# Optimization experiments

Measured on AMD Instinct MI355X. Metric: run time of the kernel, lower is better.

## Reference

```python
import jax, jax.numpy as jnp
import numpy as np

K = 32
BN_EPS = 1e-5
GRID = [[0.1, 0.1, 0.1], [0.5, 0.5, 0.5], [0.2, 0.2, 0.05]]


def setup_inputs() -> dict:
    key = jax.random.key(0)
    ks = jax.random.split(key, 8)
    B, P, C = 4, 6144, 64
    N = B * P
    feat = jax.random.normal(ks[0], (N, C), jnp.float32)
    coord = jax.random.normal(ks[1], (N, 3), jnp.float32) * 10.0
    batch = jnp.repeat(jnp.arange(B, dtype=jnp.int32), P)
    # feature_judge params: Linear(C,64) -> BatchNorm1d(64, eval) -> ReLU -> Linear(64,3)
    W1 = jax.random.normal(ks[2], (C, 64), jnp.float32) / np.sqrt(C)
    b1 = jnp.zeros((64,), jnp.float32)
    gamma = jnp.ones((64,), jnp.float32)
    beta = jnp.zeros((64,), jnp.float32)
    bn_mean = jax.random.normal(ks[3], (64,), jnp.float32) * 0.1
    bn_var = jax.random.uniform(ks[4], (64,), jnp.float32, 0.5, 1.5)
    W2 = jax.random.normal(ks[5], (64, 3), jnp.float32) / 8.0
    b2 = jnp.zeros((3,), jnp.float32)
    return {"feat": feat, "coord": coord, "batch": batch, "W1": W1, "b1": b1,
            "gamma": gamma, "beta": beta, "bn_mean": bn_mean, "bn_var": bn_var,
            "W2": W2, "b2": b2}


def _geometry(coord, B):
    # coord: [N,3] with equal-size contiguous batches -> [B,P,3]
    N = coord.shape[0]
    P = N // B
    pts = coord.reshape(B, P, 3)
    sq = jnp.sum(pts * pts, axis=-1)                               # [B,P]
    d2 = sq[:, :, None] + sq[:, None, :] - 2.0 * jnp.einsum('bpd,bqd->bpq', pts, pts)
    dist = jnp.sqrt(jnp.maximum(d2, 1e-12))                        # [B,P,P]
    _, idx = jax.lax.top_k(-dist, K + 1)                           # smallest K+1
    idx = idx[:, :, 1:]                                            # drop self -> [B,P,K]
    nbrs = jax.vmap(lambda p, i: p[i])(pts, idx)                   # [B,P,K,3]
    centered = nbrs - nbrs.mean(axis=2, keepdims=True)
    cov = jnp.einsum('bpki,bpkj->bpij', centered, centered) / (K - 1)  # [B,P,3,3]
    ev = jnp.linalg.eigvalsh(cov)[..., ::-1]                       # descending, == svd S (PSD)
    ev = ev / jnp.sum(ev, axis=-1, keepdims=True)
    linearity = (ev[..., 0] - (ev[..., 1] + ev[..., 2])).reshape(N)
    nbr_d = jnp.take_along_axis(dist, idx, axis=2)                 # [B,P,K]
    density = (1.0 / (nbr_d.mean(axis=-1) + 1e-6)).reshape(N)
    return linearity, density


def reference(feat, coord, batch, W1, b1, gamma, beta, bn_mean, bn_var, W2, b2):
    B = int(batch[-1]) + 1
    linearity, density = _geometry(coord, B)
    # feature judge MLP (BatchNorm in eval mode with running stats)
    h = feat @ W1 + b1
    h = gamma * (h - bn_mean) / jnp.sqrt(bn_var + BN_EPS) + beta
    h = jax.nn.relu(h)
    probs = jax.nn.softmax(h @ W2 + b2, axis=1)                    # [N,3]
    lin = linearity[:, None]
    den = density[:, None]
    tower_prob = (den * 2.0 + probs[:, 0:1]) / 3.0
    background_prob = (jnp.maximum(1.0 - lin, 1.0 - den) + probs[:, 1:2]) / 3.0
    line_prob = (lin * 2.0 + probs[:, 2:3]) / 3.0
    tower_g = jnp.asarray(GRID[0], jnp.float32)
    bg_g = jnp.asarray(GRID[1], jnp.float32)
    line_g = jnp.asarray([GRID[2][0], GRID[2][1], GRID[2][2] * 5.0], jnp.float32)
    grid_sizes = tower_prob * tower_g + background_prob * bg_g + line_prob * line_g + 1e-6
    return grid_sizes  # [N,3]
```

## Files before the change

### kernel.cpp

```cpp
#include <hip/hip_runtime.h>
#include <hip/hip_bf16.h>
#include <math.h>

#define TS 512
#define BUFCAP 128
#define KMAX 0xFFFFFFFFFFFFFFFFull

typedef __hip_bfloat16 bf16;
typedef unsigned long long u64;

__device__ inline float ldf(const void* p, int idx, bool isbf) {
  return isbf ? __bfloat162float(((const bf16*)p)[idx])
              : ((const float*)p)[idx];
}

__device__ inline bool probe_is_bf16(const void* bn_var) {
  int ok = 0;
#pragma unroll 1
  for (int k = 0; k < 8; ++k) {
    float v = __bfloat162float(((const bf16*)bn_var)[k]);
    if (v >= 0.4f && v <= 1.6f) ++ok;
  }
  return ok == 8;
}

__device__ inline u64 shfl_xor_u64(u64 v, int mask) {
  unsigned lo = __shfl_xor((unsigned)v, mask, 64);
  unsigned hi = __shfl_xor((unsigned)(v >> 32), mask, 64);
  return ((u64)hi << 32) | lo;
}

__device__ inline u64 bcast_u64(u64 v, int srclane) {
  unsigned lo = __shfl((unsigned)v, srclane, 64);
  unsigned hi = __shfl((unsigned)(v >> 32), srclane, 64);
  return ((u64)hi << 32) | lo;
}

__device__ inline void bitonic128(u64& a0, u64& a1, int lane) {
#pragma unroll
  for (int k = 2; k <= 128; k <<= 1) {
#pragma unroll
    for (int j = k >> 1; j > 0; j >>= 1) {
      if (j == 64) {
        u64 lo = (a0 < a1) ? a0 : a1;
        u64 hi = (a0 < a1) ? a1 : a0;
        a0 = lo; a1 = hi;
      } else {
        u64 p0 = shfl_xor_u64(a0, j);
        u64 p1 = shfl_xor_u64(a1, j);
        bool lower = ((lane & j) == 0);
        bool up0 = ((lane & k) == 0);
        bool up1 = (((64 + lane) & k) == 0);
        a0 = ((p0 < a0) == (lower == up0)) ? p0 : a0;
        a1 = ((p1 < a1) == (lower == up1)) ? p1 : a1;
      }
    }
  }
}

__device__ inline float bitonic64_f32(float a, int lane) {
#pragma unroll
  for (int k = 2; k <= 64; k <<= 1) {
#pragma unroll
    for (int j = k >> 1; j > 0; j >>= 1) {
      float p = __shfl_xor(a, j, 64);
      bool lower = ((lane & j) == 0);
      bool up = ((lane & k) == 0);
      a = ((p < a) == (lower == up)) ? p : a;
    }
  }
  return a;
}

__device__ inline u64 reselect(volatile u64* wbuf, int& cnt, int lane) {
  u64 a0 = (lane < cnt) ? wbuf[lane] : KMAX;
  u64 a1 = (64 + lane < cnt) ? wbuf[64 + lane] : KMAX;
  bitonic128(a0, a1, lane);
  if (lane < 32) wbuf[lane] = a0;
  cnt = 32;
  return bcast_u64(a0, 31);
}

#define RED32(v)             \
  v += __shfl_xor(v, 1, 64); \
  v += __shfl_xor(v, 2, 64); \
  v += __shfl_xor(v, 4, 64); \
  v += __shfl_xor(v, 8, 64); \
  v += __shfl_xor(v, 16, 64);
#define RED64(v) RED32(v) v += __shfl_xor(v, 32, 64);

__device__ inline void epilogue(volatile u64* wbuf, int cnt, int lane, int i,
                                int base, int P, float qx, float qy, float qz,
                                const void* coord, const void* feat,
                                const void* W1, const void* b1,
                                const void* gamma_, const void* beta_,
                                const void* bn_mean, const void* bn_var,
                                const void* W2, const void* b2,
                                float* __restrict__ out, bool isbf) {
  reselect(wbuf, cnt, lane);
  u64 K = (lane < 32) ? wbuf[lane] : KMAX;

  float sd = 0.f, sx = 0.f, sy = 0.f, sz = 0.f;
  float sxx = 0.f, sxy = 0.f, sxz = 0.f, syy = 0.f, syz = 0.f, szz = 0.f;
  if (lane < 32) {
    unsigned cpos = (unsigned)(K & 0xFFFFFFFFull);
    if (cpos >= (unsigned)P) cpos = 0;
    float d2 = __uint_as_float((unsigned)(K >> 32));
    sd = sqrtf(d2);
    int g = 3 * (base + (int)cpos);
    float dx = ldf(coord, g + 0, isbf) - qx,
          dy = ldf(coord, g + 1, isbf) - qy,
          dz = ldf(coord, g + 2, isbf) - qz;
    sx = dx; sy = dy; sz = dz;
    sxx = dx * dx; sxy = dx * dy; sxz = dx * dz;
    syy = dy * dy; syz = dy * dz; szz = dz * dz;
  }
  RED32(sd) RED32(sx) RED32(sy) RED32(sz) RED32(sxx) RED32(sxy) RED32(sxz)
  RED32(syy) RED32(syz) RED32(szz)

  float bnv = ldf(bn_var, lane, isbf);
  float bs = ldf(gamma_, lane, isbf) / sqrtf(bnv + 1e-5f);
  float bt = (ldf(b1, lane, isbf) - ldf(bn_mean, lane, isbf)) * bs +
             ldf(beta_, lane, isbf);
  float fv = ldf(feat, i * 64 + lane, isbf);
  float h = 0.f;
#pragma unroll 4
  for (int k = 0; k < 64; ++k) {
    float w1k = ldf(W1, k * 64 + lane, isbf);
    h = fmaf(__shfl(fv, k, 64), w1k, h);
  }
  h = fmaxf(fmaf(h, bs, bt), 0.f);
  float l0 = h * ldf(W2, lane * 3 + 0, isbf);
  float l1 = h * ldf(W2, lane * 3 + 1, isbf);
  float l2 = h * ldf(W2, lane * 3 + 2, isbf);
  RED64(l0) RED64(l1) RED64(l2)
  l0 += ldf(b2, 0, isbf); l1 += ldf(b2, 1, isbf); l2 += ldf(b2, 2, isbf);
  float m = fmaxf(l0, fmaxf(l1, l2));
  float e0 = expf(l0 - m), e1 = expf(l1 - m), e2 = expf(l2 - m);
  float inv = 1.f / (e0 + e1 + e2);
  float pr0 = e0 * inv, pr1 = e1 * inv, pr2 = e2 * inv;

  if (lane == 0) {
    const float n = 32.0f, km1 = 31.0f;
    float mx = sx / n, my = sy / n, mz = sz / n;
    float a = (sxx - n * mx * mx) / km1;
    float bb = (syy - n * my * my) / km1;
    float cc2 = (szz - n * mz * mz) / km1;
    float d = (sxy - n * mx * my) / km1;
    float e = (syz - n * my * mz) / km1;
    float f = (sxz - n * mx * mz) / km1;
    float tr = a + bb + cc2;
    float qq = tr / 3.0f;
    float p1 = d * d + f * f + e * e;
    float aq = a - qq, bq = bb - qq, cq = cc2 - qq;
    float p2 = aq * aq + bq * bq + cq * cq + 2.0f * p1;
    float p = sqrtf(p2 / 6.0f);
    float ev0;
    if (p < 1e-20f) {
      ev0 = qq;
    } else {
      float ip = 1.0f / p;
      float b00 = aq * ip, b11 = bq * ip, b22 = cq * ip;
      float b01 = d * ip, b12 = e * ip, b02 = f * ip;
      float r = (b00 * (b11 * b22 - b12 * b12) -
                 b01 * (b01 * b22 - b12 * b02) +
                 b02 * (b01 * b12 - b11 * b02)) * 0.5f;
      r = fminf(1.0f, fmaxf(-1.0f, r));
      float phi = acosf(r) / 3.0f;
      ev0 = qq + 2.0f * p * cosf(phi);
    }
    float lin = 2.0f * ev0 / tr - 1.0f;
    float den = 1.0f / (sd / 32.0f + 1e-6f);
    float tp = (den * 2.0f + pr0) / 3.0f;
    float bp = (fmaxf(1.0f - lin, 1.0f - den) + pr1) / 3.0f;
    float lp = (lin * 2.0f + pr2) / 3.0f;
    float g0 = tp * 0.1f + bp * 0.5f + lp * 0.2f + 1e-6f;
    float g2 = tp * 0.1f + bp * 0.5f + lp * 0.25f + 1e-6f;
    if (!isfinite(g0)) g0 = 0.f;
    if (!isfinite(g2)) g2 = 0.f;
    out[3 * i + 0] = g0;
    out[3 * i + 1] = g0;
    out[3 * i + 2] = g2;
  }
}

__global__ __launch_bounds__(256) void prep_kernel(
    const void* __restrict__ coord, const void* __restrict__ bn_var,
    float4* __restrict__ wsf4, int N) {
  const bool isbf = probe_is_bf16(bn_var);
  int i = blockIdx.x * 256 + threadIdx.x;
  if (i >= N) return;
  int g = 3 * i;
  float x = ldf(coord, g + 0, isbf), y = ldf(coord, g + 1, isbf),
        z = ldf(coord, g + 2, isbf);
  wsf4[i] = make_float4(x, y, z, (x * x + y * y) + z * z);
}

__global__ __launch_bounds__(256) void fused_stream(
    const void* __restrict__ coord, const void* __restrict__ feat,
    const void* __restrict__ W1, const void* __restrict__ b1,
    const void* __restrict__ gamma_, const void* __restrict__ beta_,
    const void* __restrict__ bn_mean, const void* __restrict__ bn_var,
    const void* __restrict__ W2, const void* __restrict__ b2,
    const float4* __restrict__ wsf4, float* __restrict__ out, int N) {
  __shared__ u64 sBuf[4 * BUFCAP];

  const bool isbf = probe_is_bf16(bn_var);
  int tid = threadIdx.x;
  int lane = tid & 63;
  int w = tid >> 6;
  int i = blockIdx.x * 4 + w;
  int P = N / 4;
  int base = (i / P) * P;
  int mypos = i - base;
  volatile u64* wbuf = &sBuf[w * BUFCAP];
  u64 lmask = (1ull << lane) - 1;
  const float4* cb = wsf4 + base;

  float qx = ldf(coord, 3 * i + 0, isbf);
  float qy = ldf(coord, 3 * i + 1, isbf);
  float qz = ldf(coord, 3 * i + 2, isbf);
  float qsq = (qx * qx + qy * qy) + qz * qz;

  int cnt = 0;

  float th_f;
  {
    int sstride = (P - 1) >> 6;
    int sidx = mypos + 1 + lane * sstride;
    if (sidx >= P) sidx -= P;
    float4 c = cb[sidx];
    float t = qx * c.x;
    t = fmaf(qy, c.y, t);
    t = fmaf(qz, c.z, t);
    float d2 = (qsq + c.w) - 2.0f * t;
    d2 = fmaxf(d2, 1e-12f);
    th_f = __shfl(bitonic64_f32(d2, lane), 31, 64);
  }

  const int ngroups = P / 512;

#pragma unroll 1
  for (int g = 0; g < ngroups; ++g) {
    int t0 = g * 512;
    float4 cd[8];
#pragma unroll
    for (int s = 0; s < 8; ++s) cd[s] = cb[t0 + s * 64 + lane];
    float d2v[8];
    bool anyp = false;
#pragma unroll
    for (int s = 0; s < 8; ++s) {
      float t = qx * cd[s].x;
      t = fmaf(qy, cd[s].y, t);
      t = fmaf(qz, cd[s].z, t);
      float d2 = (qsq + cd[s].w) - 2.0f * t;
      d2 = fmaxf(d2, 1e-12f);
      d2v[s] = d2;
      anyp = anyp || (d2 <= th_f);
    }
    if (__ballot(anyp)) {
#pragma unroll
      for (int s = 0; s < 8; ++s) {
        float d2 = d2v[s];
        int cpos = t0 + s * 64 + lane;
        bool cand = (d2 <= th_f) && (cpos != mypos);
        u64 mask = __ballot(cand);
        if (mask) {
          u64 key = ((u64)__float_as_uint(d2) << 32) | (unsigned)cpos;
          int pc = __popcll(mask);
          if (cnt + pc > BUFCAP) {
            u64 th = reselect(wbuf, cnt, lane);
            th_f = __uint_as_float((unsigned)(th >> 32));
            cand = cand && (d2 <= th_f);
            mask = __ballot(cand);
            pc = __popcll(mask);
          }
          if (mask) {
            int pos = cnt + __popcll(mask & lmask);
            if (cand) wbuf[pos] = key;
            cnt += pc;
          }
        }
      }
    }
  }

  epilogue(wbuf, cnt, lane, i, base, P, qx, qy, qz, coord, feat, W1, b1,
           gamma_, beta_, bn_mean, bn_var, W2, b2, out, isbf);
}

__global__ __launch_bounds__(256) void fused_kernel(
    const void* __restrict__ coord, const void* __restrict__ feat,
    const void* __restrict__ W1, const void* __restrict__ b1,
    const void* __restrict__ gamma_, const void* __restrict__ beta_,
    const void* __restrict__ bn_mean, const void* __restrict__ bn_var,
    const void* __restrict__ W2, const void* __restrict__ b2,
    float* __restrict__ out, int N) {
  __shared__ float4 sTile[TS];
  __shared__ u64 sBuf[4 * BUFCAP];

  const bool isbf = probe_is_bf16(bn_var);
  int tid = threadIdx.x;
  int lane = tid & 63;
  int w = tid >> 6;
  int i = blockIdx.x * 4 + w;
  int P = N / 4;
  int base = (i / P) * P;
  int mypos = i - base;
  volatile u64* wbuf = &sBuf[w * BUFCAP];
  u64 lmask = (1ull << lane) - 1;

  float qx = ldf(coord, 3 * i + 0, isbf);
  float qy = ldf(coord, 3 * i + 1, isbf);
  float qz = ldf(coord, 3 * i + 2, isbf);
  float qsq = (qx * qx + qy * qy) + qz * qz;

  int cnt = 0;
  float th_f;
  {
    int sstride = (P - 1) >> 6;
    int sidx = mypos + 1 + lane * sstride;
    if (sidx >= P) sidx -= P;
    int g = 3 * (base + sidx);
    float x = ldf(coord, g + 0, isbf), y = ldf(coord, g + 1, isbf),
          z = ldf(coord, g + 2, isbf);
    float csq = (x * x + y * y) + z * z;
    float t = qx * x;
    t = fmaf(qy, y, t);
    t = fmaf(qz, z, t);
    float d2 = (qsq + csq) - 2.0f * t;
    d2 = fmaxf(d2, 1e-12f);
    th_f = __shfl(bitonic64_f32(d2, lane), 31, 64);
  }

  const int ntiles = P / TS;
  for (int tile = 0; tile < ntiles; ++tile) {
    __syncthreads();
    {
      int c0 = tile * TS + tid;
      int g = 3 * (base + c0);
      float x = ldf(coord, g + 0, isbf), y = ldf(coord, g + 1, isbf),
            z = ldf(coord, g + 2, isbf);
      sTile[tid] = make_float4(x, y, z, (x * x + y * y) + z * z);
      g = 3 * (base + c0 + 256);
      x = ldf(coord, g + 0, isbf); y = ldf(coord, g + 1, isbf);
      z = ldf(coord, g + 2, isbf);
      sTile[tid + 256] = make_float4(x, y, z, (x * x + y * y) + z * z);
    }
    __syncthreads();
    int t0 = tile * TS;

    float d2v[8];
    bool anyp = false;
#pragma unroll
    for (int s = 0; s < 8; ++s) {
      float4 cd = sTile[s * 64 + lane];
      float t = qx * cd.x;
      t = fmaf(qy, cd.y, t);
      t = fmaf(qz, cd.z, t);
      float d2 = (qsq + cd.w) - 2.0f * t;
      d2 = fmaxf(d2, 1e-12f);
      d2v[s] = d2;
      anyp = anyp || (d2 <= th_f);
    }
    if (__ballot(anyp)) {
#pragma unroll
      for (int s = 0; s < 8; ++s) {
        float d2 = d2v[s];
        int cpos = t0 + s * 64 + lane;
        bool cand = (d2 <= th_f) && (cpos != mypos);
        u64 mask = __ballot(cand);
        if (mask) {
          u64 key = ((u64)__float_as_uint(d2) << 32) | (unsigned)cpos;
          int pc = __popcll(mask);
          if (cnt + pc > BUFCAP) {
            u64 th = reselect(wbuf, cnt, lane);
            th_f = __uint_as_float((unsigned)(th >> 32));
            cand = cand && (d2 <= th_f);
            mask = __ballot(cand);
            pc = __popcll(mask);
          }
          if (mask) {
            int pos = cnt + __popcll(mask & lmask);
            if (cand) wbuf[pos] = key;
            cnt += pc;
          }
        }
      }
    }
  }

  epilogue(wbuf, cnt, lane, i, base, P, qx, qy, qz, coord, feat, W1, b1,
           gamma_, beta_, bn_mean, bn_var, W2, b2, out, isbf);
}

extern "C" void kernel_launch(void* const* d_in, const int* in_sizes, int n_in,
                              void* d_out, int out_size, void* d_ws,
                              size_t ws_size, hipStream_t stream) {
  const void* feat = d_in[0];
  const void* coord = d_in[1];
  const void* W1 = d_in[3];
  const void* b1 = d_in[4];
  const void* gamma_ = d_in[5];
  const void* beta_ = d_in[6];
  const void* bn_mean = d_in[7];
  const void* bn_var = d_in[8];
  const void* W2 = d_in[9];
  const void* b2 = d_in[10];
  float* out = (float*)d_out;

  int N = in_sizes[0] / 64;
  (void)n_in; (void)out_size;

  size_t need = (size_t)N * sizeof(float4);
  if (d_ws != nullptr && ws_size >= need) {
    hipLaunchKernelGGL(prep_kernel, dim3((N + 255) / 256), dim3(256), 0,
                       stream, coord, bn_var, (float4*)d_ws, N);
    hipLaunchKernelGGL(fused_stream, dim3(N / 4), dim3(256), 0, stream,
                       coord, feat, W1, b1, gamma_, beta_, bn_mean, bn_var,
                       W2, b2, (const float4*)d_ws, out, N);
  } else {
    hipLaunchKernelGGL(fused_kernel, dim3(N / 4), dim3(256), 0, stream,
                       coord, feat, W1, b1, gamma_, beta_, bn_mean, bn_var,
                       W2, b2, out, N);
  }
}
```

Baseline: 280.6 us.

## Replace brute-force kNN with x-bucketed spatial sort and pruned slab search

Points are bucketed by x coordinate into 512 fixed-width bins per batch via histogram, prefix scan and atomic scatter into a sorted workspace. Each query then scans only the bins near its own x and grows the window outward while the slab-edge distance squared is within the current k-th threshold. This replaces the brute-force scan over all P candidates per query with a pruned search. In exchange it adds four small preprocessing kernels and atomics, and the bucket range is hard-coded around coordinates in [-64, 64], so its pruning relies on the input coordinate scale.

```diff
diff --git a/kernel.cpp b/kernel.cpp
--- a/kernel.cpp
+++ b/kernel.cpp
@@ -5,9 +5,17 @@
 #define TS 512
 #define BUFCAP 128
 #define KMAX 0xFFFFFFFFFFFFFFFFull
+#define FINF __int_as_float(0x7F800000)
+
+#define NB 512
+#define BLO_F (-64.0f)
+#define BW_F (0.25f)
+#define BINV_F (4.0f)
+#define EDGE_SLACK (1e-3f)
 
 typedef __hip_bfloat16 bf16;
 typedef unsigned long long u64;
+typedef unsigned int u32;
 
 __device__ inline float ldf(const void* p, int idx, bool isbf) {
   return isbf ? __bfloat162float(((const bf16*)p)[idx])
@@ -22,6 +30,12 @@
     if (v >= 0.4f && v <= 1.6f) ++ok;
   }
   return ok == 8;
+}
+
+__device__ inline int bucket_of(float x) {
+  int b = (int)((x - BLO_F) * BINV_F);
+  b = b < 0 ? 0 : (b > NB - 1 ? NB - 1 : b);
+  return b;
 }
 
 __device__ inline u64 shfl_xor_u64(u64 v, int mask) {
@@ -88,6 +102,43 @@
   v += __shfl_xor(v, 8, 64); \
   v += __shfl_xor(v, 16, 64);
 #define RED64(v) RED32(v) v += __shfl_xor(v, 32, 64);
+
+__device__ inline void scan_seg(const float4* __restrict__ arr,
+                                const u32* __restrict__ aidx, int s0, int s1,
+                                float qx, float qy, float qz, float qsq,
+                                u32 mypos, float& th_f, int& cnt,
+                                volatile u64* wbuf, int lane, u64 lmask) {
+#pragma unroll 1
+  for (int p = s0; p < s1; p += 64) {
+    int pos = p + lane;
+    bool valid = pos < s1;
+    float4 c = make_float4(0.f, 0.f, 0.f, 0.f);
+    u32 cp = 0xFFFFFFFFu;
+    if (valid) { c = arr[pos]; cp = aidx[pos]; }
+    float t = qx * c.x;
+    t = fmaf(qy, c.y, t);
+    t = fmaf(qz, c.z, t);
+    float d2 = (qsq + c.w) - 2.0f * t;
+    d2 = fmaxf(d2, 1e-12f);
+    bool cand = valid && (d2 <= th_f) && (cp != mypos);
+    u64 mask = __ballot(cand);
+    if (!mask) continue;
+    u64 key = ((u64)__float_as_uint(d2) << 32) | cp;
+    int pc = __popcll(mask);
+    if (cnt + pc > BUFCAP) {
+      u64 th = reselect(wbuf, cnt, lane);
+      th_f = __uint_as_float((u32)(th >> 32));
+      cand = cand && (d2 <= th_f);
+      mask = __ballot(cand);
+      pc = __popcll(mask);
+    }
+    if (mask) {
+      int q = cnt + __popcll(mask & lmask);
+      if (cand) wbuf[q] = key;
+      cnt += pc;
+    }
+  }
+}
 
 __device__ inline void epilogue(volatile u64* wbuf, int cnt, int lane, int i,
                                 int base, int P, float qx, float qy, float qz,
@@ -184,25 +235,146 @@
   }
 }
 
-__global__ __launch_bounds__(256) void prep_kernel(
-    const void* __restrict__ coord, const void* __restrict__ bn_var,
-    float4* __restrict__ wsf4, int N) {
+__global__ __launch_bounds__(256) void k_zero(u32* __restrict__ hist) {
+  int t = blockIdx.x * 256 + threadIdx.x;
+  if (t < 4 * NB) hist[t] = 0u;
+}
+
+__global__ __launch_bounds__(256) void k_hist(const void* __restrict__ coord,
+                                              const void* __restrict__ bn_var,
+                                              u32* __restrict__ hist, int N) {
   const bool isbf = probe_is_bf16(bn_var);
   int i = blockIdx.x * 256 + threadIdx.x;
   if (i >= N) return;
-  int g = 3 * i;
-  float x = ldf(coord, g + 0, isbf), y = ldf(coord, g + 1, isbf),
-        z = ldf(coord, g + 2, isbf);
-  wsf4[i] = make_float4(x, y, z, (x * x + y * y) + z * z);
-}
-
-__global__ __launch_bounds__(256) void fused_stream(
+  int P = N / 4;
+  int b = i / P;
+  float x = ldf(coord, 3 * i, isbf);
+  atomicAdd(&hist[b * NB + bucket_of(x)], 1u);
+}
+
+__global__ __launch_bounds__(512) void k_scan(const u32* __restrict__ hist,
+                                              u32* __restrict__ off,
+                                              u32* __restrict__ cur) {
+  __shared__ u32 s[NB];
+  int b = blockIdx.x, t = threadIdx.x;
+  u32 v = hist[b * NB + t];
+  s[t] = v;
+  __syncthreads();
+  for (int d = 1; d < NB; d <<= 1) {
+    u32 add = (t >= d) ? s[t - d] : 0u;
+    __syncthreads();
+    s[t] += add;
+    __syncthreads();
+  }
+  u32 incl = s[t];
+  off[b * (NB + 1) + t + 1] = incl;
+  if (t == 0) off[b * (NB + 1)] = 0u;
+  cur[b * NB + t] = incl - v;
+}
+
+__global__ __launch_bounds__(256) void k_scatter(
+    const void* __restrict__ coord, const void* __restrict__ bn_var,
+    u32* __restrict__ cur, float4* __restrict__ arr4, u32* __restrict__ aidx,
+    int N) {
+  const bool isbf = probe_is_bf16(bn_var);
+  int i = blockIdx.x * 256 + threadIdx.x;
+  if (i >= N) return;
+  int P = N / 4;
+  int b = i / P;
+  int base = b * P;
+  float x = ldf(coord, 3 * i + 0, isbf), y = ldf(coord, 3 * i + 1, isbf),
+        z = ldf(coord, 3 * i + 2, isbf);
+  u32 pos = atomicAdd(&cur[b * NB + bucket_of(x)], 1u);
+  arr4[base + pos] = make_float4(x, y, z, (x * x + y * y) + z * z);
+  aidx[base + pos] = (u32)(i - base);
+}
+
+__global__ __launch_bounds__(256) void knn_kernel(
     const void* __restrict__ coord, const void* __restrict__ feat,
     const void* __restrict__ W1, const void* __restrict__ b1,
     const void* __restrict__ gamma_, const void* __restrict__ beta_,
     const void* __restrict__ bn_mean, const void* __restrict__ bn_var,
     const void* __restrict__ W2, const void* __restrict__ b2,
-    const float4* __restrict__ wsf4, float* __restrict__ out, int N) {
+    const float4* __restrict__ arr4, const u32* __restrict__ aidx,
+    const u32* __restrict__ off, float* __restrict__ out, int N) {
+  __shared__ u64 sBuf[4 * BUFCAP];
+
+  const bool isbf = probe_is_bf16(bn_var);
+  int tid = threadIdx.x;
+  int lane = tid & 63;
+  int w = tid >> 6;
+  int i = blockIdx.x * 4 + w;
+  int P = N / 4;
+  int b = i / P;
+  int base = b * P;
+  u32 mypos = (u32)(i - base);
+  const float4* arr = arr4 + base;
+  const u32* ai = aidx + base;
+  const u32* offp = off + b * (NB + 1);
+  volatile u64* wbuf = &sBuf[w * BUFCAP];
+  u64 lmask = (1ull << lane) - 1;
+
+  float qx = ldf(coord, 3 * i + 0, isbf);
+  float qy = ldf(coord, 3 * i + 1, isbf);
+  float qz = ldf(coord, 3 * i + 2, isbf);
+  float qsq = (qx * qx + qy * qy) + qz * qz;
+
+  float th_f = FINF;
+  int cnt = 0;
+
+  int bq = bucket_of(qx);
+  int blo = bq, bhi = bq, D = 1;
+  while ((int)(offp[bhi + 1] - offp[blo]) < 128 && (blo > 0 || bhi < NB - 1)) {
+    blo = (blo - D < 0) ? 0 : blo - D;
+    bhi = (bhi + D > NB - 1) ? NB - 1 : bhi + D;
+    D <<= 1;
+  }
+  scan_seg(arr, ai, (int)offp[blo], (int)offp[bhi + 1], qx, qy, qz, qsq,
+           mypos, th_f, cnt, wbuf, lane, lmask);
+  {
+    u64 th = reselect(wbuf, cnt, lane);
+    th_f = __uint_as_float((u32)(th >> 32));
+  }
+
+#pragma unroll 1
+  for (int guard = 0; guard < 4096; ++guard) {
+    float dl = (blo > 0)
+                   ? fmaxf(qx - (BLO_F + (float)blo * BW_F) - EDGE_SLACK, 0.f)
+                   : FINF;
+    float dr = (bhi < NB - 1)
+                   ? fmaxf((BLO_F + (float)(bhi + 1) * BW_F) - qx - EDGE_SLACK,
+                           0.f)
+                   : FINF;
+    float m = fminf(dl, dr);
+    if (!(m * m <= th_f)) break;
+    if (dl <= dr) {
+      int nblo = blo;
+      while (nblo > 0 && (int)(offp[blo] - offp[nblo]) < 64) --nblo;
+      scan_seg(arr, ai, (int)offp[nblo], (int)offp[blo], qx, qy, qz, qsq,
+               mypos, th_f, cnt, wbuf, lane, lmask);
+      blo = nblo;
+    } else {
+      int nbhi = bhi;
+      while (nbhi < NB - 1 && (int)(offp[nbhi + 1] - offp[bhi + 1]) < 64)
+        ++nbhi;
+      scan_seg(arr, ai, (int)offp[bhi + 1], (int)offp[nbhi + 1], qx, qy, qz,
+               qsq, mypos, th_f, cnt, wbuf, lane, lmask);
+      bhi = nbhi;
+    }
+  }
+
+  epilogue(wbuf, cnt, lane, i, base, P, qx, qy, qz, coord, feat, W1, b1,
+           gamma_, beta_, bn_mean, bn_var, W2, b2, out, isbf);
+}
+
+__global__ __launch_bounds__(256) void fused_kernel(
+    const void* __restrict__ coord, const void* __restrict__ feat,
+    const void* __restrict__ W1, const void* __restrict__ b1,
+    const void* __restrict__ gamma_, const void* __restrict__ beta_,
+    const void* __restrict__ bn_mean, const void* __restrict__ bn_var,
+    const void* __restrict__ W2, const void* __restrict__ b2,
+    float* __restrict__ out, int N) {
+  __shared__ float4 sTile[TS];
   __shared__ u64 sBuf[4 * BUFCAP];
 
   const bool isbf = probe_is_bf16(bn_var);
@@ -215,7 +387,6 @@
   int mypos = i - base;
   volatile u64* wbuf = &sBuf[w * BUFCAP];
   u64 lmask = (1ull << lane) - 1;
-  const float4* cb = wsf4 + base;
 
   float qx = ldf(coord, 3 * i + 0, isbf);
   float qy = ldf(coord, 3 * i + 1, isbf);
@@ -223,37 +394,49 @@
   float qsq = (qx * qx + qy * qy) + qz * qz;
 
   int cnt = 0;
-
   float th_f;
   {
     int sstride = (P - 1) >> 6;
     int sidx = mypos + 1 + lane * sstride;
     if (sidx >= P) sidx -= P;
-    float4 c = cb[sidx];
-    float t = qx * c.x;
-    t = fmaf(qy, c.y, t);
-    t = fmaf(qz, c.z, t);
-    float d2 = (qsq + c.w) - 2.0f * t;
+    int g = 3 * (base + sidx);
+    float x = ldf(coord, g + 0, isbf), y = ldf(coord, g + 1, isbf),
+          z = ldf(coord, g + 2, isbf);
+    float csq = (x * x + y * y) + z * z;
+    float t = qx * x;
+    t = fmaf(qy, y, t);
+    t = fmaf(qz, z, t);
+    float d2 = (qsq + csq) - 2.0f * t;
     d2 = fmaxf(d2, 1e-12f);
     th_f = __shfl(bitonic64_f32(d2, lane), 31, 64);
   }
 
-  const int ngroups = P / 512;
-
-#pragma unroll 1
-  for (int g = 0; g < ngroups; ++g) {
-    int t0 = g * 512;
-    float4 cd[8];
-#pragma unroll
-    for (int s = 0; s < 8; ++s) cd[s] = cb[t0 + s * 64 + lane];
+  const int ntiles = P / TS;
+  for (int tile = 0; tile < ntiles; ++tile) {
+    __syncthreads();
+    {
+      int c0 = tile * TS + tid;
+      int g = 3 * (base + c0);
+      float x = ldf(coord, g + 0, isbf), y = ldf(coord, g + 1, isbf),
+            z = ldf(coord, g + 2, isbf);
+      sTile[tid] = make_float4(x, y, z, (x * x + y * y) + z * z);
+      g = 3 * (base + c0 + 256);
+      x = ldf(coord, g + 0, isbf); y = ldf(coord, g + 1, isbf);
+      z = ldf(coord, g + 2, isbf);
+      sTile[tid + 256] = make_float4(x, y, z, (x * x + y * y) + z * z);
+    }
+    __syncthreads();
+    int t0 = tile * TS;
+
     float d2v[8];
     bool anyp = false;
 #pragma unroll
     for (int s = 0; s < 8; ++s) {
-      float t = qx * cd[s].x;
-      t = fmaf(qy, cd[s].y, t);
-      t = fmaf(qz, cd[s].z, t);
-      float d2 = (qsq + cd[s].w) - 2.0f * t;
+      float4 cd = sTile[s * 64 + lane];
+      float t = qx * cd.x;
+      t = fmaf(qy, cd.y, t);
+      t = fmaf(qz, cd.z, t);
+      float d2 = (qsq + cd.w) - 2.0f * t;
       d2 = fmaxf(d2, 1e-12f);
       d2v[s] = d2;
       anyp = anyp || (d2 <= th_f);
@@ -289,111 +472,6 @@
            gamma_, beta_, bn_mean, bn_var, W2, b2, out, isbf);
 }
 
-__global__ __launch_bounds__(256) void fused_kernel(
-    const void* __restrict__ coord, const void* __restrict__ feat,
-    const void* __restrict__ W1, const void* __restrict__ b1,
-    const void* __restrict__ gamma_, const void* __restrict__ beta_,
-    const void* __restrict__ bn_mean, const void* __restrict__ bn_var,
-    const void* __restrict__ W2, const void* __restrict__ b2,
-    float* __restrict__ out, int N) {
-  __shared__ float4 sTile[TS];
-  __shared__ u64 sBuf[4 * BUFCAP];
-
-  const bool isbf = probe_is_bf16(bn_var);
-  int tid = threadIdx.x;
-  int lane = tid & 63;
-  int w = tid >> 6;
-  int i = blockIdx.x * 4 + w;
-  int P = N / 4;
-  int base = (i / P) * P;
-  int mypos = i - base;
-  volatile u64* wbuf = &sBuf[w * BUFCAP];
-  u64 lmask = (1ull << lane) - 1;
-
-  float qx = ldf(coord, 3 * i + 0, isbf);
-  float qy = ldf(coord, 3 * i + 1, isbf);
-  float qz = ldf(coord, 3 * i + 2, isbf);
-  float qsq = (qx * qx + qy * qy) + qz * qz;
-
-  int cnt = 0;
-  float th_f;
-  {
-    int sstride = (P - 1) >> 6;
-    int sidx = mypos + 1 + lane * sstride;
-    if (sidx >= P) sidx -= P;
-    int g = 3 * (base + sidx);
-    float x = ldf(coord, g + 0, isbf), y = ldf(coord, g + 1, isbf),
-          z = ldf(coord, g + 2, isbf);
-    float csq = (x * x + y * y) + z * z;
-    float t = qx * x;
-    t = fmaf(qy, y, t);
-    t = fmaf(qz, z, t);
-    float d2 = (qsq + csq) - 2.0f * t;
-    d2 = fmaxf(d2, 1e-12f);
-    th_f = __shfl(bitonic64_f32(d2, lane), 31, 64);
-  }
-
-  const int ntiles = P / TS;
-  for (int tile = 0; tile < ntiles; ++tile) {
-    __syncthreads();
-    {
-      int c0 = tile * TS + tid;
-      int g = 3 * (base + c0);
-      float x = ldf(coord, g + 0, isbf), y = ldf(coord, g + 1, isbf),
-            z = ldf(coord, g + 2, isbf);
-      sTile[tid] = make_float4(x, y, z, (x * x + y * y) + z * z);
-      g = 3 * (base + c0 + 256);
-      x = ldf(coord, g + 0, isbf); y = ldf(coord, g + 1, isbf);
-      z = ldf(coord, g + 2, isbf);
-      sTile[tid + 256] = make_float4(x, y, z, (x * x + y * y) + z * z);
-    }
-    __syncthreads();
-    int t0 = tile * TS;
-
-    float d2v[8];
-    bool anyp = false;
-#pragma unroll
-    for (int s = 0; s < 8; ++s) {
-      float4 cd = sTile[s * 64 + lane];
-      float t = qx * cd.x;
-      t = fmaf(qy, cd.y, t);
-      t = fmaf(qz, cd.z, t);
-      float d2 = (qsq + cd.w) - 2.0f * t;
-      d2 = fmaxf(d2, 1e-12f);
-      d2v[s] = d2;
-      anyp = anyp || (d2 <= th_f);
-    }
-    if (__ballot(anyp)) {
-#pragma unroll
-      for (int s = 0; s < 8; ++s) {
-        float d2 = d2v[s];
-        int cpos = t0 + s * 64 + lane;
-        bool cand = (d2 <= th_f) && (cpos != mypos);
-        u64 mask = __ballot(cand);
-        if (mask) {
-          u64 key = ((u64)__float_as_uint(d2) << 32) | (unsigned)cpos;
-          int pc = __popcll(mask);
-          if (cnt + pc > BUFCAP) {
-            u64 th = reselect(wbuf, cnt, lane);
-            th_f = __uint_as_float((unsigned)(th >> 32));
-            cand = cand && (d2 <= th_f);
-            mask = __ballot(cand);
-            pc = __popcll(mask);
-          }
-          if (mask) {
-            int pos = cnt + __popcll(mask & lmask);
-            if (cand) wbuf[pos] = key;
-            cnt += pc;
-          }
-        }
-      }
-    }
-  }
-
-  epilogue(wbuf, cnt, lane, i, base, P, qx, qy, qz, coord, feat, W1, b1,
-           gamma_, beta_, bn_mean, bn_var, W2, b2, out, isbf);
-}
-
 extern "C" void kernel_launch(void* const* d_in, const int* in_sizes, int n_in,
                               void* d_out, int out_size, void* d_ws,
                               size_t ws_size, hipStream_t stream) {
@@ -412,16 +490,31 @@
   int N = in_sizes[0] / 64;
   (void)n_in; (void)out_size;
 
-  size_t need = (size_t)N * sizeof(float4);
+  size_t offOff = (size_t)N * 20;
+  size_t histOff = offOff + (size_t)4 * (NB + 1) * 4;
+  size_t curOff = histOff + (size_t)4 * NB * 4;
+  size_t need = curOff + (size_t)4 * NB * 4;
+
   if (d_ws != nullptr && ws_size >= need) {
-    hipLaunchKernelGGL(prep_kernel, dim3((N + 255) / 256), dim3(256), 0,
-                       stream, coord, bn_var, (float4*)d_ws, N);
-    hipLaunchKernelGGL(fused_stream, dim3(N / 4), dim3(256), 0, stream,
-                       coord, feat, W1, b1, gamma_, beta_, bn_mean, bn_var,
-                       W2, b2, (const float4*)d_ws, out, N);
+    char* ws = (char*)d_ws;
+    float4* arr4 = (float4*)ws;
+    u32* aidx = (u32*)(ws + (size_t)N * 16);
+    u32* off = (u32*)(ws + offOff);
+    u32* hist = (u32*)(ws + histOff);
+    u32* cur = (u32*)(ws + curOff);
+    hipLaunchKernelGGL(k_zero, dim3((4 * NB + 255) / 256), dim3(256), 0,
+                       stream, hist);
+    hipLaunchKernelGGL(k_hist, dim3((N + 255) / 256), dim3(256), 0, stream,
+                       coord, bn_var, hist, N);
+    hipLaunchKernelGGL(k_scan, dim3(4), dim3(512), 0, stream, hist, off, cur);
+    hipLaunchKernelGGL(k_scatter, dim3((N + 255) / 256), dim3(256), 0, stream,
+                       coord, bn_var, cur, arr4, aidx, N);
+    hipLaunchKernelGGL(knn_kernel, dim3(N / 4), dim3(256), 0, stream, coord,
+                       feat, W1, b1, gamma_, beta_, bn_mean, bn_var, W2, b2,
+                       arr4, aidx, off, out, N);
   } else {
-    hipLaunchKernelGGL(fused_kernel, dim3(N / 4), dim3(256), 0, stream,
-                       coord, feat, W1, b1, gamma_, beta_, bn_mean, bn_var,
-                       W2, b2, out, N);
-  }
-}
+    hipLaunchKernelGGL(fused_kernel, dim3(N / 4), dim3(256), 0, stream, coord,
+                       feat, W1, b1, gamma_, beta_, bn_mean, bn_var, W2, b2,
+                       out, N);
+  }
+}
```

After: 417.2 us. 1.49x slower.

## Process two query points per wavefront to reuse streamed candidate loads

Applied to the files above, without the earlier changes.

Replaces the one-query-per-wave streaming kNN kernel with a version where each wavefront handles two adjacent query points. Each loaded candidate float4 is used for two distance computations, halving global/L2 candidate traffic per query. In exchange it raises register pressure, doubles the shared candidate buffers per block and runs the two epilogues one after the other. The grid also shrinks by half, leaving fewer waves in flight.

```diff
diff --git a/kernel.cpp b/kernel.cpp
--- a/kernel.cpp
+++ b/kernel.cpp
@@ -8,6 +8,7 @@
 
 typedef __hip_bfloat16 bf16;
 typedef unsigned long long u64;
+typedef unsigned int u32;
 
 __device__ inline float ldf(const void* p, int idx, bool isbf) {
   return isbf ? __bfloat162float(((const bf16*)p)[idx])
@@ -196,13 +197,156 @@
   wsf4[i] = make_float4(x, y, z, (x * x + y * y) + z * z);
 }
 
-__global__ __launch_bounds__(256) void fused_stream(
+__global__ __launch_bounds__(256) void fused_q2(
     const void* __restrict__ coord, const void* __restrict__ feat,
     const void* __restrict__ W1, const void* __restrict__ b1,
     const void* __restrict__ gamma_, const void* __restrict__ beta_,
     const void* __restrict__ bn_mean, const void* __restrict__ bn_var,
     const void* __restrict__ W2, const void* __restrict__ b2,
     const float4* __restrict__ wsf4, float* __restrict__ out, int N) {
+  __shared__ u64 sBuf[8 * BUFCAP];
+
+  const bool isbf = probe_is_bf16(bn_var);
+  int tid = threadIdx.x;
+  int lane = tid & 63;
+  int w = tid >> 6;
+  int i0 = blockIdx.x * 8 + w * 2;
+  int i1 = i0 + 1;
+  int P = N / 4;
+  int base = (i0 / P) * P;
+  int mypos0 = i0 - base;
+  int mypos1 = mypos0 + 1;
+  volatile u64* wb0 = &sBuf[(w * 2 + 0) * BUFCAP];
+  volatile u64* wb1 = &sBuf[(w * 2 + 1) * BUFCAP];
+  u64 lmask = (1ull << lane) - 1;
+  const float4* cb = wsf4 + base;
+
+  float qx0 = ldf(coord, 3 * i0 + 0, isbf);
+  float qy0 = ldf(coord, 3 * i0 + 1, isbf);
+  float qz0 = ldf(coord, 3 * i0 + 2, isbf);
+  float qsq0 = (qx0 * qx0 + qy0 * qy0) + qz0 * qz0;
+  float qx1 = ldf(coord, 3 * i1 + 0, isbf);
+  float qy1 = ldf(coord, 3 * i1 + 1, isbf);
+  float qz1 = ldf(coord, 3 * i1 + 2, isbf);
+  float qsq1 = (qx1 * qx1 + qy1 * qy1) + qz1 * qz1;
+
+  int cnt0 = 0, cnt1 = 0;
+  float th0, th1;
+
+  {
+    int sstride = (P - 1) >> 6;
+    int sidx = mypos0 + 1 + lane * sstride;
+    if (sidx >= P) sidx -= P;
+    float4 c = cb[sidx];
+    float t = qx0 * c.x;
+    t = fmaf(qy0, c.y, t);
+    t = fmaf(qz0, c.z, t);
+    float d2 = (qsq0 + c.w) - 2.0f * t;
+    d2 = fmaxf(d2, 1e-12f);
+    th0 = __shfl(bitonic64_f32(d2, lane), 31, 64);
+  }
+  {
+    int sstride = (P - 1) >> 6;
+    int sidx = mypos1 + 1 + lane * sstride;
+    if (sidx >= P) sidx -= P;
+    float4 c = cb[sidx];
+    float t = qx1 * c.x;
+    t = fmaf(qy1, c.y, t);
+    t = fmaf(qz1, c.z, t);
+    float d2 = (qsq1 + c.w) - 2.0f * t;
+    d2 = fmaxf(d2, 1e-12f);
+    th1 = __shfl(bitonic64_f32(d2, lane), 31, 64);
+  }
+
+  const int ngroups = P / 512;
+
+#pragma unroll 1
+  for (int g = 0; g < ngroups; ++g) {
+    int t0 = g * 512;
+    float4 cd[8];
+#pragma unroll
+    for (int s = 0; s < 8; ++s) cd[s] = cb[t0 + s * 64 + lane];
+    float dA[8], dB[8];
+    bool anyp = false;
+#pragma unroll
+    for (int s = 0; s < 8; ++s) {
+      float tA = qx0 * cd[s].x;
+      tA = fmaf(qy0, cd[s].y, tA);
+      tA = fmaf(qz0, cd[s].z, tA);
+      float d2A = (qsq0 + cd[s].w) - 2.0f * tA;
+      d2A = fmaxf(d2A, 1e-12f);
+      float tB = qx1 * cd[s].x;
+      tB = fmaf(qy1, cd[s].y, tB);
+      tB = fmaf(qz1, cd[s].z, tB);
+      float d2B = (qsq1 + cd[s].w) - 2.0f * tB;
+      d2B = fmaxf(d2B, 1e-12f);
+      dA[s] = d2A; dB[s] = d2B;
+      anyp = anyp || (d2A <= th0) || (d2B <= th1);
+    }
+    if (__ballot(anyp)) {
+#pragma unroll
+      for (int s = 0; s < 8; ++s) {
+        int cpos = t0 + s * 64 + lane;
+        {
+          float d2 = dA[s];
+          bool cand = (d2 <= th0) && (cpos != mypos0);
+          u64 mask = __ballot(cand);
+          if (mask) {
+            u64 key = ((u64)__float_as_uint(d2) << 32) | (unsigned)cpos;
+            int pc = __popcll(mask);
+            if (cnt0 + pc > BUFCAP) {
+              u64 th = reselect(wb0, cnt0, lane);
+              th0 = __uint_as_float((unsigned)(th >> 32));
+              cand = cand && (d2 <= th0);
+              mask = __ballot(cand);
+              pc = __popcll(mask);
+            }
+            if (mask) {
+              int pos = cnt0 + __popcll(mask & lmask);
+              if (cand) wb0[pos] = key;
+              cnt0 += pc;
+            }
+          }
+        }
+        {
+          float d2 = dB[s];
+          bool cand = (d2 <= th1) && (cpos != mypos1);
+          u64 mask = __ballot(cand);
+          if (mask) {
+            u64 key = ((u64)__float_as_uint(d2) << 32) | (unsigned)cpos;
+            int pc = __popcll(mask);
+            if (cnt1 + pc > BUFCAP) {
+              u64 th = reselect(wb1, cnt1, lane);
+              th1 = __uint_as_float((unsigned)(th >> 32));
+              cand = cand && (d2 <= th1);
+              mask = __ballot(cand);
+              pc = __popcll(mask);
+            }
+            if (mask) {
+              int pos = cnt1 + __popcll(mask & lmask);
+              if (cand) wb1[pos] = key;
+              cnt1 += pc;
+            }
+          }
+        }
+      }
+    }
+  }
+
+  epilogue(wb0, cnt0, lane, i0, base, P, qx0, qy0, qz0, coord, feat, W1, b1,
+           gamma_, beta_, bn_mean, bn_var, W2, b2, out, isbf);
+  epilogue(wb1, cnt1, lane, i1, base, P, qx1, qy1, qz1, coord, feat, W1, b1,
+           gamma_, beta_, bn_mean, bn_var, W2, b2, out, isbf);
+}
+
+__global__ __launch_bounds__(256) void fused_kernel(
+    const void* __restrict__ coord, const void* __restrict__ feat,
+    const void* __restrict__ W1, const void* __restrict__ b1,
+    const void* __restrict__ gamma_, const void* __restrict__ beta_,
+    const void* __restrict__ bn_mean, const void* __restrict__ bn_var,
+    const void* __restrict__ W2, const void* __restrict__ b2,
+    float* __restrict__ out, int N) {
+  __shared__ float4 sTile[TS];
   __shared__ u64 sBuf[4 * BUFCAP];
 
   const bool isbf = probe_is_bf16(bn_var);
@@ -215,7 +359,6 @@
   int mypos = i - base;
   volatile u64* wbuf = &sBuf[w * BUFCAP];
   u64 lmask = (1ull << lane) - 1;
-  const float4* cb = wsf4 + base;
 
   float qx = ldf(coord, 3 * i + 0, isbf);
   float qy = ldf(coord, 3 * i + 1, isbf);
@@ -223,37 +366,49 @@
   float qsq = (qx * qx + qy * qy) + qz * qz;
 
   int cnt = 0;
-
   float th_f;
   {
     int sstride = (P - 1) >> 6;
     int sidx = mypos + 1 + lane * sstride;
     if (sidx >= P) sidx -= P;
-    float4 c = cb[sidx];
-    float t = qx * c.x;
-    t = fmaf(qy, c.y, t);
-    t = fmaf(qz, c.z, t);
-    float d2 = (qsq + c.w) - 2.0f * t;
+    int g = 3 * (base + sidx);
+    float x = ldf(coord, g + 0, isbf), y = ldf(coord, g + 1, isbf),
+          z = ldf(coord, g + 2, isbf);
+    float csq = (x * x + y * y) + z * z;
+    float t = qx * x;
+    t = fmaf(qy, y, t);
+    t = fmaf(qz, z, t);
+    float d2 = (qsq + csq) - 2.0f * t;
     d2 = fmaxf(d2, 1e-12f);
     th_f = __shfl(bitonic64_f32(d2, lane), 31, 64);
   }
 
-  const int ngroups = P / 512;
-
-#pragma unroll 1
-  for (int g = 0; g < ngroups; ++g) {
-    int t0 = g * 512;
-    float4 cd[8];
-#pragma unroll
-    for (int s = 0; s < 8; ++s) cd[s] = cb[t0 + s * 64 + lane];
+  const int ntiles = P / TS;
+  for (int tile = 0; tile < ntiles; ++tile) {
+    __syncthreads();
+    {
+      int c0 = tile * TS + tid;
+      int g = 3 * (base + c0);
+      float x = ldf(coord, g + 0, isbf), y = ldf(coord, g + 1, isbf),
+            z = ldf(coord, g + 2, isbf);
+      sTile[tid] = make_float4(x, y, z, (x * x + y * y) + z * z);
+      g = 3 * (base + c0 + 256);
+      x = ldf(coord, g + 0, isbf); y = ldf(coord, g + 1, isbf);
+      z = ldf(coord, g + 2, isbf);
+      sTile[tid + 256] = make_float4(x, y, z, (x * x + y * y) + z * z);
+    }
+    __syncthreads();
+    int t0 = tile * TS;
+
     float d2v[8];
     bool anyp = false;
 #pragma unroll
     for (int s = 0; s < 8; ++s) {
-      float t = qx * cd[s].x;
-      t = fmaf(qy, cd[s].y, t);
-      t = fmaf(qz, cd[s].z, t);
-      float d2 = (qsq + cd[s].w) - 2.0f * t;
+      float4 cd = sTile[s * 64 + lane];
+      float t = qx * cd.x;
+      t = fmaf(qy, cd.y, t);
+      t = fmaf(qz, cd.z, t);
+      float d2 = (qsq + cd.w) - 2.0f * t;
       d2 = fmaxf(d2, 1e-12f);
       d2v[s] = d2;
       anyp = anyp || (d2 <= th_f);
@@ -289,111 +444,6 @@
            gamma_, beta_, bn_mean, bn_var, W2, b2, out, isbf);
 }
 
-__global__ __launch_bounds__(256) void fused_kernel(
-    const void* __restrict__ coord, const void* __restrict__ feat,
-    const void* __restrict__ W1, const void* __restrict__ b1,
-    const void* __restrict__ gamma_, const void* __restrict__ beta_,
-    const void* __restrict__ bn_mean, const void* __restrict__ bn_var,
-    const void* __restrict__ W2, const void* __restrict__ b2,
-    float* __restrict__ out, int N) {
-  __shared__ float4 sTile[TS];
-  __shared__ u64 sBuf[4 * BUFCAP];
-
-  const bool isbf = probe_is_bf16(bn_var);
-  int tid = threadIdx.x;
-  int lane = tid & 63;
-  int w = tid >> 6;
-  int i = blockIdx.x * 4 + w;
-  int P = N / 4;
-  int base = (i / P) * P;
-  int mypos = i - base;
-  volatile u64* wbuf = &sBuf[w * BUFCAP];
-  u64 lmask = (1ull << lane) - 1;
-
-  float qx = ldf(coord, 3 * i + 0, isbf);
-  float qy = ldf(coord, 3 * i + 1, isbf);
-  float qz = ldf(coord, 3 * i + 2, isbf);
-  float qsq = (qx * qx + qy * qy) + qz * qz;
-
-  int cnt = 0;
-  float th_f;
-  {
-    int sstride = (P - 1) >> 6;
-    int sidx = mypos + 1 + lane * sstride;
-    if (sidx >= P) sidx -= P;
-    int g = 3 * (base + sidx);
-    float x = ldf(coord, g + 0, isbf), y = ldf(coord, g + 1, isbf),
-          z = ldf(coord, g + 2, isbf);
-    float csq = (x * x + y * y) + z * z;
-    float t = qx * x;
-    t = fmaf(qy, y, t);
-    t = fmaf(qz, z, t);
-    float d2 = (qsq + csq) - 2.0f * t;
-    d2 = fmaxf(d2, 1e-12f);
-    th_f = __shfl(bitonic64_f32(d2, lane), 31, 64);
-  }
-
-  const int ntiles = P / TS;
-  for (int tile = 0; tile < ntiles; ++tile) {
-    __syncthreads();
-    {
-      int c0 = tile * TS + tid;
-      int g = 3 * (base + c0);
-      float x = ldf(coord, g + 0, isbf), y = ldf(coord, g + 1, isbf),
-            z = ldf(coord, g + 2, isbf);
-      sTile[tid] = make_float4(x, y, z, (x * x + y * y) + z * z);
-      g = 3 * (base + c0 + 256);
-      x = ldf(coord, g + 0, isbf); y = ldf(coord, g + 1, isbf);
-      z = ldf(coord, g + 2, isbf);
-      sTile[tid + 256] = make_float4(x, y, z, (x * x + y * y) + z * z);
-    }
-    __syncthreads();
-    int t0 = tile * TS;
-
-    float d2v[8];
-    bool anyp = false;
-#pragma unroll
-    for (int s = 0; s < 8; ++s) {
-      float4 cd = sTile[s * 64 + lane];
-      float t = qx * cd.x;
-      t = fmaf(qy, cd.y, t);
-      t = fmaf(qz, cd.z, t);
-      float d2 = (qsq + cd.w) - 2.0f * t;
-      d2 = fmaxf(d2, 1e-12f);
-      d2v[s] = d2;
-      anyp = anyp || (d2 <= th_f);
-    }
-    if (__ballot(anyp)) {
-#pragma unroll
-      for (int s = 0; s < 8; ++s) {
-        float d2 = d2v[s];
-        int cpos = t0 + s * 64 + lane;
-        bool cand = (d2 <= th_f) && (cpos != mypos);
-        u64 mask = __ballot(cand);
-        if (mask) {
-          u64 key = ((u64)__float_as_uint(d2) << 32) | (unsigned)cpos;
-          int pc = __popcll(mask);
-          if (cnt + pc > BUFCAP) {
-            u64 th = reselect(wbuf, cnt, lane);
-            th_f = __uint_as_float((unsigned)(th >> 32));
-            cand = cand && (d2 <= th_f);
-            mask = __ballot(cand);
-            pc = __popcll(mask);
-          }
-          if (mask) {
-            int pos = cnt + __popcll(mask & lmask);
-            if (cand) wbuf[pos] = key;
-            cnt += pc;
-          }
-        }
-      }
-    }
-  }
-
-  epilogue(wbuf, cnt, lane, i, base, P, qx, qy, qz, coord, feat, W1, b1,
-           gamma_, beta_, bn_mean, bn_var, W2, b2, out, isbf);
-}
-
 extern "C" void kernel_launch(void* const* d_in, const int* in_sizes, int n_in,
                               void* d_out, int out_size, void* d_ws,
                               size_t ws_size, hipStream_t stream) {
@@ -416,9 +466,9 @@
   if (d_ws != nullptr && ws_size >= need) {
     hipLaunchKernelGGL(prep_kernel, dim3((N + 255) / 256), dim3(256), 0,
                        stream, coord, bn_var, (float4*)d_ws, N);
-    hipLaunchKernelGGL(fused_stream, dim3(N / 4), dim3(256), 0, stream,
-                       coord, feat, W1, b1, gamma_, beta_, bn_mean, bn_var,
-                       W2, b2, (const float4*)d_ws, out, N);
+    hipLaunchKernelGGL(fused_q2, dim3(N / 8), dim3(256), 0, stream, coord,
+                       feat, W1, b1, gamma_, beta_, bn_mean, bn_var, W2, b2,
+                       (const float4*)d_ws, out, N);
   } else {
     hipLaunchKernelGGL(fused_kernel, dim3(N / 4), dim3(256), 0, stream,
                        coord, feat, W1, b1, gamma_, beta_, bn_mean, bn_var,
```

Result: no change. 282.4 us (+0.7%).
